# Performance work log

Measured on AMD Instinct MI355X. Metric: run time of the kernel, lower is better.

The kernel has to match this reference:

```python
import jax, jax.numpy as jnp
import numpy as np

DIM = 768
HEADS = 8
FRAMES = 9
B, T, N = 16, FRAMES, 1024
HEAD_DIM = DIM // HEADS
SCALE = HEAD_DIM ** -0.5


def setup_inputs() -> dict:
    key = jax.random.key(0)
    ks = jax.random.split(key, 6)
    s = lambda fan_in: 1.0 / np.sqrt(fan_in)
    return {
        "x": jax.random.normal(ks[0], (B, T, N, DIM), jnp.float32),
        "W_qkv": jax.random.normal(ks[1], (DIM, 3 * DIM), jnp.float32) * s(DIM),
        "W_temp": jax.random.normal(ks[2], (T, T), jnp.float32) * s(T),
        "b_temp": jax.random.normal(ks[3], (T,), jnp.float32) * s(T),
        "W_out": jax.random.normal(ks[4], (DIM, DIM), jnp.float32) * s(DIM),
        "b_out": jax.random.normal(ks[5], (DIM,), jnp.float32) * s(DIM),
    }


def reference(x, W_qkv, W_temp, b_temp, W_out, b_out):
    b, t, n, c = x.shape
    h, d = HEADS, HEAD_DIM
    qkv = x @ W_qkv  # (b,t,n,3c)
    q, k, v = jnp.split(qkv, 3, axis=-1)
    # 'b t n (h d) -> b h t n d'
    to_heads = lambda a: a.reshape(b, t, n, h, d).transpose(0, 3, 1, 2, 4)
    q, k, v = to_heads(q), to_heads(k), to_heads(v)
    # dots over d per spatial token, then mean over n: fuse mean into the contraction
    dots = jnp.einsum('bhtnd,bhsnd->bhts', q, k) * (SCALE / n)  # (b,h,t,s)
    attn = jax.nn.softmax(dots, axis=-1)
    # temporal_proj(attn.mean over heads): Linear on last dim s
    ta = attn.mean(axis=1) @ W_temp + b_temp  # (b,t,s)
    # broadcast over h,n,d: out[b,h,t,n,d] = sum_s ta[b,t,s] * v[b,h,s,n,d]
    out = jnp.einsum('bts,bhsnd->bhtnd', ta, v)
    out = out.transpose(0, 2, 3, 1, 4).reshape(b, t, n, c)  # 'b h t n d -> b t n (h d)'
    return out @ W_out + b_out
```

## Files before the change

### kernel.cpp

```cpp
#include <hip/hip_runtime.h>
#include <stdint.h>

typedef unsigned short u16;
typedef float f32x4 __attribute__((ext_vector_type(4)));
typedef short s16x8 __attribute__((ext_vector_type(8)));
typedef unsigned short u16x4 __attribute__((ext_vector_type(4)));

#define NB 16
#define NT 9
#define NN 1024
#define NDIM 768
#define NH 8
#define NHD 96
#define NM (NB*NT*NN)
#define NQK 1536
#define PLANE (NN*NDIM)
#define SCALE_F 0.10206207261596575f

typedef __attribute__((address_space(1))) const void gvoid_t;
typedef __attribute__((address_space(3))) void lvoid_t;
#define GLOAD_LDS16(gp, lp) __builtin_amdgcn_global_load_lds((gvoid_t*)(gp), (lvoid_t*)(lp), 16, 0, 0)

__device__ __forceinline__ size_t gpack(int row, int col) {
    return (size_t)(row >> 4) * 12288 + ((col >> 5) * 512)
         + (((row & 15) + 16 * ((col >> 3) & 3)) * 8) + (col & 7);
}

__device__ __forceinline__ unsigned f2bf_u(float x) {
    unsigned u = __builtin_bit_cast(unsigned, x);
    return (u + 0x7FFFu + ((u >> 16) & 1u)) >> 16;
}
__device__ __forceinline__ void cvt8(uint4 v, float* f) {
    f[0] = __builtin_bit_cast(float, v.x << 16);
    f[1] = __builtin_bit_cast(float, v.x & 0xFFFF0000u);
    f[2] = __builtin_bit_cast(float, v.y << 16);
    f[3] = __builtin_bit_cast(float, v.y & 0xFFFF0000u);
    f[4] = __builtin_bit_cast(float, v.z << 16);
    f[5] = __builtin_bit_cast(float, v.z & 0xFFFF0000u);
    f[6] = __builtin_bit_cast(float, v.w << 16);
    f[7] = __builtin_bit_cast(float, v.w & 0xFFFF0000u);
}
__device__ __forceinline__ uint4 pack8(const float* f) {
    uint4 o;
    o.x = f2bf_u(f[0]) | (f2bf_u(f[1]) << 16);
    o.y = f2bf_u(f[2]) | (f2bf_u(f[3]) << 16);
    o.z = f2bf_u(f[4]) | (f2bf_u(f[5]) << 16);
    o.w = f2bf_u(f[6]) | (f2bf_u(f[7]) << 16);
    return o;
}

__global__ void wqk_pack(const float* __restrict__ Wqkv, u16* __restrict__ BP) {
    int j = blockIdx.x * 32 + threadIdx.x;
    int c = blockIdx.y * 32 + threadIdx.y;
    BP[gpack(j, c)] = (u16)f2bf_u(Wqkv[(size_t)c * 2304 + j]);
}

__global__ void wvo_gemm(const float* __restrict__ Wqkv, const float* __restrict__ Wout,
                         u16* __restrict__ BPo) {
    __shared__ float la[32][33];
    __shared__ float lb[32][33];
    int c0 = blockIdx.x * 32, c20 = blockIdx.y * 32;
    int tx = threadIdx.x, ty = threadIdx.y;
    float acc = 0.f;
    for (int e0 = 0; e0 < 768; e0 += 32) {
        la[ty][tx] = Wout[(size_t)(e0 + ty) * 768 + c20 + tx];
        lb[ty][tx] = Wqkv[(size_t)(c0 + ty) * 2304 + 1536 + e0 + tx];
        __syncthreads();
        #pragma unroll
        for (int e = 0; e < 32; ++e)
            acc = fmaf(la[e][ty], lb[tx][e], acc);
        __syncthreads();
    }
    BPo[gpack(c20 + ty, c0 + tx)] = (u16)f2bf_u(acc);
}

__global__ __launch_bounds__(256)
void cvt_pack_x(const float* __restrict__ x, u16* __restrict__ xb) {
    const int g  = blockIdx.x;
    const int bt = blockIdx.y;
    const float* src = x + (size_t)bt * PLANE;
    u16* dst = xb + (size_t)bt * PLANE + (size_t)g * 12288;
    #pragma unroll 1
    for (int s = threadIdx.x; s < 1536; s += 256) {
        int nl = s / 96, cc = s % 96;
        const float* sp = src + ((size_t)(g * 16 + nl)) * 768 + cc * 8;
        float f[8];
        f32x4 v0 = *(const f32x4*)sp;
        f32x4 v1 = *(const f32x4*)(sp + 4);
        f[0] = v0.x; f[1] = v0.y; f[2] = v0.z; f[3] = v0.w;
        f[4] = v1.x; f[5] = v1.y; f[6] = v1.z; f[7] = v1.w;
        int off = (cc >> 2) * 512 + (nl + 16 * (cc & 3)) * 8;
        *(uint4*)(dst + off) = pack8(f);
    }
}

template<int WM>
__global__ __launch_bounds__(512, 2)
void gemm256(const u16* __restrict__ A, const u16* __restrict__ BP,
             void* __restrict__ Cv, const float* __restrict__ bias, int N) {
    constexpr int KT = 24;
    __shared__ __align__(16) u16 lA[4 * 8192];
    const int tid  = threadIdx.x;
    const int lane = tid & 63;
    const int wid  = tid >> 6;
    const int wr   = wid >> 2;
    const int wc   = wid & 3;
    const int nbx  = N >> 8;
    const int cpx  = (int)gridDim.x >> 3;
    const int bid  = (int)blockIdx.x;
    const int swzb = (bid & 7) * cpx + (bid >> 3);
    const int bx   = swzb % nbx, by = swzb / nbx;
    const long m0  = (long)by << 8;
    const long n0  = (long)bx << 8;
    const int  g0  = (int)(m0 >> 4);

    const u16* ag0 = A + (size_t)(g0 + wid) * 12288 + lane * 8;
    const u16* ag1 = ag0 + (size_t)8 * 12288;
    u16* ad0 = lA + wid * 512;
    u16* ad1 = ad0 + 4096;
    const u16* bg[4];
    #pragma unroll
    for (int ni = 0; ni < 4; ++ni)
        bg[ni] = BP + (size_t)((n0 >> 4) + wc * 4 + ni) * 12288 + lane * 8;

    f32x4 acc[8][4] = {};
    s16x8 bf[2][4];

    #define STAGE(tt) { GLOAD_LDS16(ag0 + (tt) * 512, ad0 + ((tt) & 3) * 8192); \
                        GLOAD_LDS16(ag1 + (tt) * 512, ad1 + ((tt) & 3) * 8192); }

    #pragma unroll
    for (int ni = 0; ni < 4; ++ni) bf[0][ni] = *(const s16x8*)(bg[ni]);
    STAGE(0); STAGE(1);
    asm volatile("s_waitcnt vmcnt(2)" ::: "memory");
    __builtin_amdgcn_s_barrier();

    #pragma unroll 2
    for (int t = 0; t < KT; ++t) {
        const u16* lp = lA + (t & 3) * 8192;
        s16x8 af[8];
        #pragma unroll
        for (int mi = 0; mi < 8; ++mi)
            af[mi] = *(const s16x8*)(lp + (wr * 8 + mi) * 512 + lane * 8);
        if (t + 1 < KT) {
            #pragma unroll
            for (int ni = 0; ni < 4; ++ni)
                bf[(t + 1) & 1][ni] = *(const s16x8*)(bg[ni] + (t + 1) * 512);
        }
        if (t + 2 < KT) STAGE(t + 2);
        __builtin_amdgcn_s_setprio(1);
        #pragma unroll
        for (int mi = 0; mi < 8; ++mi)
            #pragma unroll
            for (int ni = 0; ni < 4; ++ni)
                acc[mi][ni] = __builtin_amdgcn_mfma_f32_16x16x32_bf16(
                    af[mi], bf[t & 1][ni], acc[mi][ni], 0, 0, 0);
        __builtin_amdgcn_s_setprio(0);
        asm volatile("s_waitcnt vmcnt(6)" ::: "memory");
        __builtin_amdgcn_s_barrier();
    }
    #undef STAGE

    const int crow = (lane >> 4) << 2;
    const int ccol = lane & 15;
    if constexpr (WM == 0) {
        u16* C = (u16*)Cv;
        #pragma unroll
        for (int mi = 0; mi < 8; ++mi)
            #pragma unroll
            for (int ni = 0; ni < 4; ++ni) {
                long r = m0 + wr * 128 + mi * 16 + crow;
                long c = n0 + wc * 64 + ni * 16 + ccol;
                #pragma unroll
                for (int i = 0; i < 4; ++i)
                    C[(r + i) * (long)N + c] = (u16)f2bf_u(acc[mi][ni][i]);
            }
    } else {
        float* C = (float*)Cv;
        #pragma unroll
        for (int mi = 0; mi < 8; ++mi)
            #pragma unroll
            for (int ni = 0; ni < 4; ++ni) {
                long r = m0 + wr * 128 + mi * 16 + crow;
                long c = n0 + wc * 64 + ni * 16 + ccol;
                float bv = bias[c];
                #pragma unroll
                for (int i = 0; i < 4; ++i)
                    C[(r + i) * (long)N + c] = acc[mi][ni][i] + bv;
            }
    }
}

__global__ __launch_bounds__(256)
void dots_partial(const u16* __restrict__ QK, float* __restrict__ part) {
    const int tid = threadIdx.x;
    const int ch  = blockIdx.x;
    const int h   = blockIdx.y;
    const int b   = blockIdx.z;
    const size_t tstride = (size_t)NN * NQK;
    const u16* base = QK + (size_t)b * 9 * tstride + h * NHD;

    float acc[9][9] = {};
    #pragma unroll 1
    for (int j = 0; j < 3; ++j) {
        int p  = ch * 768 + j * 256 + tid;
        int n  = p / 12, dc = p % 12;
        const u16* qp = base + (size_t)n * NQK + dc * 8;
        float qf[9][8];
        #pragma unroll
        for (int t = 0; t < 9; ++t) {
            uint4 qv = *(const uint4*)(qp + (size_t)t * tstride);
            cvt8(qv, qf[t]);
        }
        #pragma unroll
        for (int s = 0; s < 9; ++s) {
            uint4 kv = *(const uint4*)(qp + (size_t)s * tstride + 768);
            float kf[8]; cvt8(kv, kf);
            #pragma unroll
            for (int t = 0; t < 9; ++t)
                #pragma unroll
                for (int e = 0; e < 8; ++e)
                    acc[t][s] = fmaf(qf[t][e], kf[e], acc[t][s]);
        }
    }
    #pragma unroll
    for (int t = 0; t < 9; ++t)
        #pragma unroll
        for (int s = 0; s < 9; ++s) {
            float v = acc[t][s];
            #pragma unroll
            for (int m = 1; m < 64; m <<= 1) v += __shfl_xor(v, m, 64);
            acc[t][s] = v;
        }
    __shared__ float red[4][81];
    if ((tid & 63) == 0) {
        #pragma unroll
        for (int t = 0; t < 9; ++t)
            #pragma unroll
            for (int s = 0; s < 9; ++s) red[tid >> 6][t * 9 + s] = acc[t][s];
    }
    __syncthreads();
    if (tid < 81) {
        float v = red[0][tid] + red[1][tid] + red[2][tid] + red[3][tid];
        part[((size_t)ch * 128 + b * 8 + h) * 81 + tid] = v;
    }
}

__global__ void finalize_ta(const float* __restrict__ part, const float* __restrict__ Wtmp,
                            const float* __restrict__ btmp, float* __restrict__ ta) {
    const int b = blockIdx.x;
    const int tid = threadIdx.x;
    __shared__ float attn_l[8][9][9];
    if (tid < 72) {
        int h = tid / 9, t = tid % 9;
        float v[9];
        #pragma unroll
        for (int s = 0; s < 9; ++s) {
            float a = 0.f;
            for (int ch = 0; ch < 16; ++ch)
                a += part[((size_t)ch * 128 + b * 8 + h) * 81 + t * 9 + s];
            v[s] = a * (SCALE_F / 1024.0f);
        }
        float mx = v[0];
        #pragma unroll
        for (int s = 1; s < 9; ++s) mx = fmaxf(mx, v[s]);
        float den = 0.f;
        #pragma unroll
        for (int s = 0; s < 9; ++s) { v[s] = __expf(v[s] - mx); den += v[s]; }
        float inv = 1.0f / den;
        #pragma unroll
        for (int s = 0; s < 9; ++s) attn_l[h][t][s] = v[s] * inv;
    }
    __syncthreads();
    if (tid < 81) {
        int t = tid / 9, j = tid % 9;
        float o = btmp[j];
        #pragma unroll
        for (int s = 0; s < 9; ++s) {
            float am = 0.f;
            #pragma unroll
            for (int hh = 0; hh < 8; ++hh) am += attn_l[hh][t][s];
            o = fmaf(am * 0.125f, Wtmp[s * 9 + j], o);
        }
        ta[(size_t)b * 81 + t * 9 + j] = o;
    }
}

__global__ __launch_bounds__(256)
void tmix(u16* __restrict__ xb, const float* __restrict__ ta) {
    const int b = blockIdx.y;
    const int tid = threadIdx.x;
    __shared__ float tl[81];
    if (tid < 81) tl[tid] = ta[(size_t)b * 81 + tid];
    __syncthreads();
    size_t off = ((size_t)blockIdx.x * 256 + tid) * 8;
    u16* pb = xb + (size_t)b * 9 * PLANE + off;
    float acc[9][8] = {};
    #pragma unroll
    for (int s = 0; s < 9; ++s) {
        uint4 xv = *(const uint4*)(pb + (size_t)s * PLANE);
        float xf[8]; cvt8(xv, xf);
        #pragma unroll
        for (int t = 0; t < 9; ++t) {
            float w = tl[t * 9 + s];
            #pragma unroll
            for (int e = 0; e < 8; ++e) acc[t][e] = fmaf(w, xf[e], acc[t][e]);
        }
    }
    #pragma unroll
    for (int t = 0; t < 9; ++t)
        *(uint4*)(pb + (size_t)t * PLANE) = pack8(acc[t]);
}

extern "C" void kernel_launch(void* const* d_in, const int* in_sizes, int n_in,
                              void* d_out, int out_size, void* d_ws, size_t ws_size,
                              hipStream_t stream) {
    (void)in_sizes; (void)n_in; (void)out_size; (void)ws_size;
    const float* x    = (const float*)d_in[0];
    const float* Wqkv = (const float*)d_in[1];
    const float* Wtmp = (const float*)d_in[2];
    const float* btmp = (const float*)d_in[3];
    const float* Wout = (const float*)d_in[4];
    const float* bout = (const float*)d_in[5];

    char* ws = (char*)d_ws;
    u16*   xb   = (u16*)ws;
    u16*   BPqk = (u16*)(ws + 226492416ull);
    u16*   BPo  = (u16*)(ws + 228851712ull);
    float* part = (float*)(ws + 230031360ull);
    float* ta   = (float*)(ws + 230694912ull);
    u16*   QK   = (u16*)d_out;

    wqk_pack<<<dim3(48, 24), dim3(32, 32), 0, stream>>>(Wqkv, BPqk);
    wvo_gemm<<<dim3(24, 24), dim3(32, 32), 0, stream>>>(Wqkv, Wout, BPo);
    cvt_pack_x<<<dim3(64, 144), 256, 0, stream>>>(x, xb);
    gemm256<0><<<3456, 512, 0, stream>>>(xb, BPqk, (void*)QK, nullptr, NQK);
    dots_partial<<<dim3(16, 8, 16), 256, 0, stream>>>(QK, part);
    finalize_ta<<<16, 128, 0, stream>>>(part, Wtmp, btmp, ta);
    tmix<<<dim3(384, 16), 256, 0, stream>>>(xb, ta);
    gemm256<1><<<1728, 512, 0, stream>>>(xb, BPo, d_out, bout, NDIM);
}
```

Before: 1.240 ms.

## Shrink GEMM tiles to 256x128 with LDS-staged B and store QK in fp8

The shared GEMM kernel moves from a 256x256 tile, where B was read from global into registers, to a 256x128 tile. Both A and B are now staged through a three-buffer LDS ring with async global-to-LDS loads, and the launch bound targets four blocks per SM. The Q/K projection output is now written as fp8 instead of bf16 and decoded with packed fp8 conversions in the dots reduction. This halves the intermediate traffic for that reduction. The fp8 storage lowers the precision of the attention logits and could threaten accuracy, and the smaller tile reloads A more often.

```diff
diff --git a/kernel.cpp b/kernel.cpp
--- a/kernel.cpp
+++ b/kernel.cpp
@@ -2,7 +2,9 @@
 #include <stdint.h>
 
 typedef unsigned short u16;
+typedef unsigned char u8;
 typedef float f32x4 __attribute__((ext_vector_type(4)));
+typedef float f32x2 __attribute__((ext_vector_type(2)));
 typedef short s16x8 __attribute__((ext_vector_type(8)));
 typedef unsigned short u16x4 __attribute__((ext_vector_type(4)));
 
@@ -47,6 +49,14 @@
     o.z = f2bf_u(f[4]) | (f2bf_u(f[5]) << 16);
     o.w = f2bf_u(f[6]) | (f2bf_u(f[7]) << 16);
     return o;
+}
+__device__ __forceinline__ void dec8(uint2 v, float* f) {
+    f32x2 a0 = __builtin_amdgcn_cvt_pk_f32_fp8(v.x, false);
+    f32x2 a1 = __builtin_amdgcn_cvt_pk_f32_fp8(v.x, true);
+    f32x2 a2 = __builtin_amdgcn_cvt_pk_f32_fp8(v.y, false);
+    f32x2 a3 = __builtin_amdgcn_cvt_pk_f32_fp8(v.y, true);
+    f[0] = a0[0]; f[1] = a0[1]; f[2] = a1[0]; f[3] = a1[1];
+    f[4] = a2[0]; f[5] = a2[1]; f[6] = a3[0]; f[7] = a3[1];
 }
 
 __global__ void wqk_pack(const float* __restrict__ Wqkv, u16* __restrict__ BP) {
@@ -95,68 +105,64 @@
 }
 
 template<int WM>
-__global__ __launch_bounds__(512, 2)
+__global__ __launch_bounds__(512, 4)
 void gemm256(const u16* __restrict__ A, const u16* __restrict__ BP,
              void* __restrict__ Cv, const float* __restrict__ bias, int N) {
     constexpr int KT = 24;
-    __shared__ __align__(16) u16 lA[4 * 8192];
+    __shared__ __align__(16) u16 lds[3 * 12288];
     const int tid  = threadIdx.x;
     const int lane = tid & 63;
     const int wid  = tid >> 6;
-    const int wr   = wid >> 2;
-    const int wc   = wid & 3;
-    const int nbx  = N >> 8;
+    const int wm   = wid >> 1;
+    const int wn   = wid & 1;
+    const int nbx  = N >> 7;
     const int cpx  = (int)gridDim.x >> 3;
     const int bid  = (int)blockIdx.x;
     const int swzb = (bid & 7) * cpx + (bid >> 3);
     const int bx   = swzb % nbx, by = swzb / nbx;
     const long m0  = (long)by << 8;
-    const long n0  = (long)bx << 8;
+    const long n0  = (long)bx << 7;
     const int  g0  = (int)(m0 >> 4);
-
-    const u16* ag0 = A + (size_t)(g0 + wid) * 12288 + lane * 8;
-    const u16* ag1 = ag0 + (size_t)8 * 12288;
-    u16* ad0 = lA + wid * 512;
-    u16* ad1 = ad0 + 4096;
-    const u16* bg[4];
-    #pragma unroll
-    for (int ni = 0; ni < 4; ++ni)
-        bg[ni] = BP + (size_t)((n0 >> 4) + wc * 4 + ni) * 12288 + lane * 8;
-
-    f32x4 acc[8][4] = {};
-    s16x8 bf[2][4];
-
-    #define STAGE(tt) { GLOAD_LDS16(ag0 + (tt) * 512, ad0 + ((tt) & 3) * 8192); \
-                        GLOAD_LDS16(ag1 + (tt) * 512, ad1 + ((tt) & 3) * 8192); }
-
-    #pragma unroll
-    for (int ni = 0; ni < 4; ++ni) bf[0][ni] = *(const s16x8*)(bg[ni]);
+    const int  h0  = (int)(n0 >> 4);
+
+    const u16* agp0 = A  + (size_t)(g0 + wid) * 12288 + lane * 8;
+    const u16* agp1 = A  + (size_t)(g0 + wid + 8) * 12288 + lane * 8;
+    const u16* bgp  = BP + (size_t)(h0 + wid) * 12288 + lane * 8;
+    u16* adp0 = lds + wid * 512;
+    u16* adp1 = lds + (wid + 8) * 512;
+    u16* bdp  = lds + 8192 + wid * 512;
+
+    f32x4 acc[4][4] = {};
+
+    #define STAGE(tt) { const int o_ = ((tt) % 3) * 12288; const int k_ = (tt) * 512; \
+        GLOAD_LDS16(agp0 + k_, adp0 + o_); GLOAD_LDS16(agp1 + k_, adp1 + o_); \
+        GLOAD_LDS16(bgp  + k_, bdp  + o_); }
+
     STAGE(0); STAGE(1);
-    asm volatile("s_waitcnt vmcnt(2)" ::: "memory");
+    asm volatile("s_waitcnt vmcnt(3)" ::: "memory");
     __builtin_amdgcn_s_barrier();
 
-    #pragma unroll 2
+    #pragma unroll 3
     for (int t = 0; t < KT; ++t) {
-        const u16* lp = lA + (t & 3) * 8192;
-        s16x8 af[8];
-        #pragma unroll
-        for (int mi = 0; mi < 8; ++mi)
-            af[mi] = *(const s16x8*)(lp + (wr * 8 + mi) * 512 + lane * 8);
-        if (t + 1 < KT) {
-            #pragma unroll
-            for (int ni = 0; ni < 4; ++ni)
-                bf[(t + 1) & 1][ni] = *(const s16x8*)(bg[ni] + (t + 1) * 512);
-        }
+        const u16* lp = lds + (t % 3) * 12288;
+        s16x8 af[4], bf[4];
+        #pragma unroll
+        for (int mi = 0; mi < 4; ++mi)
+            af[mi] = *(const s16x8*)(lp + (wm * 4 + mi) * 512 + lane * 8);
+        #pragma unroll
+        for (int ni = 0; ni < 4; ++ni)
+            bf[ni] = *(const s16x8*)(lp + 8192 + (wn * 4 + ni) * 512 + lane * 8);
         if (t + 2 < KT) STAGE(t + 2);
         __builtin_amdgcn_s_setprio(1);
         #pragma unroll
-        for (int mi = 0; mi < 8; ++mi)
+        for (int mi = 0; mi < 4; ++mi)
             #pragma unroll
             for (int ni = 0; ni < 4; ++ni)
                 acc[mi][ni] = __builtin_amdgcn_mfma_f32_16x16x32_bf16(
-                    af[mi], bf[t & 1][ni], acc[mi][ni], 0, 0, 0);
+                    af[mi], bf[ni], acc[mi][ni], 0, 0, 0);
         __builtin_amdgcn_s_setprio(0);
-        asm volatile("s_waitcnt vmcnt(6)" ::: "memory");
+        if (t <= KT - 3)      { asm volatile("s_waitcnt vmcnt(3)" ::: "memory"); }
+        else if (t == KT - 2) { asm volatile("s_waitcnt vmcnt(0)" ::: "memory"); }
         __builtin_amdgcn_s_barrier();
     }
     #undef STAGE
@@ -164,25 +170,28 @@
     const int crow = (lane >> 4) << 2;
     const int ccol = lane & 15;
     if constexpr (WM == 0) {
-        u16* C = (u16*)Cv;
-        #pragma unroll
-        for (int mi = 0; mi < 8; ++mi)
+        u8* C = (u8*)Cv;
+        #pragma unroll
+        for (int mi = 0; mi < 4; ++mi)
             #pragma unroll
             for (int ni = 0; ni < 4; ++ni) {
-                long r = m0 + wr * 128 + mi * 16 + crow;
-                long c = n0 + wc * 64 + ni * 16 + ccol;
+                long r = m0 + wm * 64 + mi * 16 + crow;
+                long c = n0 + wn * 64 + ni * 16 + ccol;
                 #pragma unroll
-                for (int i = 0; i < 4; ++i)
-                    C[(r + i) * (long)N + c] = (u16)f2bf_u(acc[mi][ni][i]);
+                for (int i = 0; i < 4; ++i) {
+                    unsigned pk = __builtin_amdgcn_cvt_pk_fp8_f32(
+                        acc[mi][ni][i], acc[mi][ni][i], 0, false);
+                    C[(r + i) * (long)N + c] = (u8)(pk & 0xFF);
+                }
             }
     } else {
         float* C = (float*)Cv;
         #pragma unroll
-        for (int mi = 0; mi < 8; ++mi)
+        for (int mi = 0; mi < 4; ++mi)
             #pragma unroll
             for (int ni = 0; ni < 4; ++ni) {
-                long r = m0 + wr * 128 + mi * 16 + crow;
-                long c = n0 + wc * 64 + ni * 16 + ccol;
+                long r = m0 + wm * 64 + mi * 16 + crow;
+                long c = n0 + wn * 64 + ni * 16 + ccol;
                 float bv = bias[c];
                 #pragma unroll
                 for (int i = 0; i < 4; ++i)
@@ -192,30 +201,30 @@
 }
 
 __global__ __launch_bounds__(256)
-void dots_partial(const u16* __restrict__ QK, float* __restrict__ part) {
+void dots_partial(const u8* __restrict__ QK, float* __restrict__ part) {
     const int tid = threadIdx.x;
     const int ch  = blockIdx.x;
     const int h   = blockIdx.y;
     const int b   = blockIdx.z;
     const size_t tstride = (size_t)NN * NQK;
-    const u16* base = QK + (size_t)b * 9 * tstride + h * NHD;
+    const u8* base = QK + (size_t)b * 9 * tstride + h * NHD;
 
     float acc[9][9] = {};
     #pragma unroll 1
     for (int j = 0; j < 3; ++j) {
         int p  = ch * 768 + j * 256 + tid;
         int n  = p / 12, dc = p % 12;
-        const u16* qp = base + (size_t)n * NQK + dc * 8;
+        const u8* qp = base + (size_t)n * NQK + dc * 8;
         float qf[9][8];
         #pragma unroll
         for (int t = 0; t < 9; ++t) {
-            uint4 qv = *(const uint4*)(qp + (size_t)t * tstride);
-            cvt8(qv, qf[t]);
+            uint2 qv = *(const uint2*)(qp + (size_t)t * tstride);
+            dec8(qv, qf[t]);
         }
         #pragma unroll
         for (int s = 0; s < 9; ++s) {
-            uint4 kv = *(const uint4*)(qp + (size_t)s * tstride + 768);
-            float kf[8]; cvt8(kv, kf);
+            uint2 kv = *(const uint2*)(qp + (size_t)s * tstride + 768);
+            float kf[8]; dec8(kv, kf);
             #pragma unroll
             for (int t = 0; t < 9; ++t)
                 #pragma unroll
@@ -329,14 +338,14 @@
     u16*   BPo  = (u16*)(ws + 228851712ull);
     float* part = (float*)(ws + 230031360ull);
     float* ta   = (float*)(ws + 230694912ull);
-    u16*   QK   = (u16*)d_out;
+    u8*    QK8  = (u8*)d_out;
 
     wqk_pack<<<dim3(48, 24), dim3(32, 32), 0, stream>>>(Wqkv, BPqk);
     wvo_gemm<<<dim3(24, 24), dim3(32, 32), 0, stream>>>(Wqkv, Wout, BPo);
     cvt_pack_x<<<dim3(64, 144), 256, 0, stream>>>(x, xb);
-    gemm256<0><<<3456, 512, 0, stream>>>(xb, BPqk, (void*)QK, nullptr, NQK);
-    dots_partial<<<dim3(16, 8, 16), 256, 0, stream>>>(QK, part);
+    gemm256<0><<<6912, 512, 0, stream>>>(xb, BPqk, (void*)QK8, nullptr, NQK);
+    dots_partial<<<dim3(16, 8, 16), 256, 0, stream>>>(QK8, part);
     finalize_ta<<<16, 128, 0, stream>>>(part, Wtmp, btmp, ta);
     tmix<<<dim3(384, 16), 256, 0, stream>>>(xb, ta);
-    gemm256<1><<<1728, 512, 0, stream>>>(xb, BPo, d_out, bout, NDIM);
-}
+    gemm256<1><<<3456, 512, 0, stream>>>(xb, BPo, d_out, bout, NDIM);
+}
```

Result: slower. 1.494 ms (+20.5%).
